# Kernel tuning notes

Measured on AMD Instinct MI355X. Metric: run time of the kernel, lower is better.

## Reference

```python
import math
import jax, jax.numpy as jnp
import numpy as np

B, S, M, H = 8, 2048, 2048, 512
GH = 512  # gate_hidden
MIX_BIAS = -0.25
VARIATION_BIAS = -1.0
PRIOR_SCALE = 1.0
GATE_SCALE = 1.0
GATE_BIAS = 0.0
EPS = 1e-6


def _slerp(a, b, t, eps=EPS):
    # F.normalize semantics: x / max(||x||, eps)
    an = a / jnp.maximum(jnp.linalg.norm(a, axis=-1, keepdims=True), eps)
    bn = b / jnp.maximum(jnp.linalg.norm(b, axis=-1, keepdims=True), eps)
    dot = jnp.clip(jnp.sum(an * bn, axis=-1, keepdims=True), -1.0 + eps, 1.0 - eps)
    omega = jnp.arccos(dot)
    sin_omega = jnp.maximum(jnp.sin(omega), eps)
    t = jnp.clip(t, 0.0, 1.0)
    scale_a = jnp.sin((1.0 - t) * omega) / sin_omega
    scale_b = jnp.sin(t * omega) / sin_omega
    return scale_a * a + scale_b * b


def setup_inputs() -> dict:
    key = jax.random.key(0)
    ks = jax.random.split(key, 20)
    sc = 1.0 / math.sqrt(H)
    sc4 = 1.0 / math.sqrt(4 * H)
    scg = 1.0 / math.sqrt(GH)
    inp = {
        "query": jax.random.normal(ks[0], (B, S, H), jnp.float32),
        "global_anchor": jax.random.normal(ks[1], (B, H), jnp.float32),
        "global_memory": jax.random.normal(ks[2], (B, M, H), jnp.float32),
        "local_absolute": jax.random.normal(ks[3], (B, S, H), jnp.float32),
        "style_context": jax.random.normal(ks[4], (B, S, H), jnp.float32),
        # projection params, stored as [in, out]
        "Wq": jax.random.normal(ks[5], (H, H), jnp.float32) * sc,
        "bq": jnp.zeros((H,), jnp.float32),
        "Wk": jax.random.normal(ks[6], (H, H), jnp.float32) * sc,
        "bk": jnp.zeros((H,), jnp.float32),
        "Wv": jax.random.normal(ks[7], (H, H), jnp.float32) * sc,
        "bv": jnp.zeros((H,), jnp.float32),
        "Wo": jax.random.normal(ks[8], (H, H), jnp.float32) * sc,
        "bo": jnp.zeros((H,), jnp.float32),
        # mix gate MLP: 4H -> GH -> 1
        "Wm1": jax.random.normal(ks[9], (4 * H, GH), jnp.float32) * sc4,
        "bm1": jnp.zeros((GH,), jnp.float32),
        "Wm2": jax.random.normal(ks[10], (GH, 1), jnp.float32) * scg,
        "bm2": jnp.zeros((1,), jnp.float32),
        # variation gate MLP: 4H -> GH -> 1
        "Wg1": jax.random.normal(ks[11], (4 * H, GH), jnp.float32) * sc4,
        "bg1": jnp.zeros((GH,), jnp.float32),
        "Wg2": jax.random.normal(ks[12], (GH, 1), jnp.float32) * scg,
        "bg2": jnp.zeros((1,), jnp.float32),
    }
    return inp


def reference(query, global_anchor, global_memory, local_absolute, style_context,
              Wq, bq, Wk, bk, Wv, bv, Wo, bo,
              Wm1, bm1, Wm2, bm2, Wg1, bg1, Wg2, bg2):
    # expand anchor [B,H] -> [B,S,H]
    anchor_seq = jnp.broadcast_to(global_anchor[:, None, :], query.shape)

    q = query @ Wq + bq                      # [B,S,H]
    k = global_memory @ Wk + bk              # [B,M,H]
    v = global_memory @ Wv + bv              # [B,M,H]

    attn_logits = jnp.einsum('bsh,bmh->bsm', q, k) / math.sqrt(float(H))
    attn = jax.nn.softmax(attn_logits, axis=-1)                      # [B,S,M]
    prior_delta = (jnp.einsum('bsm,bmh->bsh', attn, v) @ Wo + bo) * PRIOR_SCALE
    prior_absolute = anchor_seq + prior_delta

    mix_in = jnp.concatenate([query, prior_absolute, local_absolute, style_context], axis=-1)
    mix_logit = jax.nn.relu(mix_in @ Wm1 + bm1) @ Wm2 + bm2          # [B,S,1]
    mix = jax.nn.sigmoid(mix_logit + MIX_BIAS)

    candidate_absolute = _slerp(prior_absolute, local_absolute, mix)

    var_in = jnp.concatenate([query, candidate_absolute, anchor_seq, style_context], axis=-1)
    variation_logit = jax.nn.relu(var_in @ Wg1 + bg1) @ Wg2 + bg2    # [B,S,1]
    variation_gate = jax.nn.sigmoid(variation_logit * GATE_SCALE + GATE_BIAS + VARIATION_BIAS)

    candidate_delta = candidate_absolute - anchor_seq
    return (attn, prior_delta, prior_absolute, mix, candidate_absolute,
            candidate_delta, variation_logit, variation_gate)
```

## Files before the change

kernel.cpp:

```cpp
#include <hip/hip_runtime.h>
#include <hip/hip_bf16.h>

typedef __hip_bfloat16 bf16;
typedef unsigned short u16;
typedef u16 u16x8 __attribute__((ext_vector_type(8)));
typedef u16 u16x4v __attribute__((ext_vector_type(4)));
typedef short bf16x8 __attribute__((ext_vector_type(8)));
typedef float f32x4 __attribute__((ext_vector_type(4)));

__device__ __forceinline__ float b2f(u16 u) {
    unsigned v = ((unsigned)u) << 16;
    float f; __builtin_memcpy(&f, &v, 4); return f;
}
__device__ __forceinline__ u16 f2u(float f) {
    bf16 h = __float2bfloat16(f);
    u16 u; __builtin_memcpy(&u, &h, 2); return u;
}
__device__ __forceinline__ float sigmoidf_(float x) { return 1.f / (1.f + expf(-x)); }
__device__ __forceinline__ void load8f(const float* __restrict__ p, float* x) {
    float4 a = *reinterpret_cast<const float4*>(p);
    float4 b = *reinterpret_cast<const float4*>(p + 4);
    x[0]=a.x; x[1]=a.y; x[2]=a.z; x[3]=a.w; x[4]=b.x; x[5]=b.y; x[6]=b.z; x[7]=b.w;
}

__device__ __forceinline__ void gld16(const void* g, void* l) {
    typedef __attribute__((address_space(1))) const unsigned int GU;
    typedef __attribute__((address_space(3))) unsigned int LU;
    __builtin_amdgcn_global_load_lds((GU*)(unsigned long long)g,
                                     (LU*)(unsigned int)(unsigned long long)l, 16, 0, 0);
}

template<int EPI, int SWZ>
__global__ __launch_bounds__(256)
void k_mfma(const bf16* __restrict__ A, long long sA, int lda,
            const bf16* __restrict__ Bt, long long sB, int ldb,
            const float* __restrict__ bias,
            bf16* __restrict__ outb, long long sO,
            float* __restrict__ out1, float* __restrict__ out2,
            const float* __restrict__ anchor,
            int N, int K, float scale, int GX)
{
    __shared__ short As[4096];
    __shared__ short Bs[4096];
    const int tid = threadIdx.x;
    const int lin = blockIdx.x;
    int x, y, z;
    if constexpr (SWZ == 0) {
        z = lin & 7; const int t = lin >> 3; x = t % GX; y = t / GX;
    } else {
        const int q = (int)gridDim.x >> 3;
        const int wq = (lin & 7) * q + (lin >> 3);
        x = wq % GX; y = wq / GX; z = 0;
    }
    const int n0 = x * 128, m0 = y * 128;
    const bf16* Az = A + (long long)z * sA;
    const bf16* Bz = Bt + (long long)z * sB;
    const int lrow = tid >> 2;
    const int lcol = (tid & 3) * 8;
    const int lane = tid & 63, w = tid >> 6;
    const int wm = (w >> 1) * 64, wn = (w & 1) * 64;
    const int fr = lane & 15, fq = lane >> 4;
    char* AsW = (char*)As + w * 1024;
    char* BsW = (char*)Bs + w * 1024;

    f32x4 acc[4][4];
#pragma unroll
    for (int i = 0; i < 4; ++i)
#pragma unroll
        for (int j = 0; j < 4; ++j) acc[i][j] = f32x4{0.f, 0.f, 0.f, 0.f};

    for (int k0 = 0; k0 < K; k0 += 32) {
        const bf16* ga = Az + (long long)(m0 + lrow) * lda + (k0 + lcol);
        const bf16* gb = Bz + (long long)(n0 + lrow) * ldb + (k0 + lcol);
        gld16(ga, AsW);
        gld16(ga + 64LL * lda, AsW + 4096);
        gld16(gb, BsW);
        gld16(gb + 64LL * ldb, BsW + 4096);
        __syncthreads();

        bf16x8 af[4], bfr[4];
#pragma unroll
        for (int i = 0; i < 4; ++i)
            af[i] = *reinterpret_cast<const bf16x8*>(&As[(wm + i * 16 + fr) * 32 + fq * 8]);
#pragma unroll
        for (int j = 0; j < 4; ++j)
            bfr[j] = *reinterpret_cast<const bf16x8*>(&Bs[(wn + j * 16 + fr) * 32 + fq * 8]);
#pragma unroll
        for (int i = 0; i < 4; ++i)
#pragma unroll
            for (int j = 0; j < 4; ++j)
                acc[i][j] = __builtin_amdgcn_mfma_f32_16x16x32_bf16(af[i], bfr[j], acc[i][j], 0, 0, 0);
        __syncthreads();
    }

#pragma unroll
    for (int j = 0; j < 4; ++j) {
        const int col = n0 + wn + j * 16 + fr;
        const float bv = bias ? bias[col] : 0.f;
#pragma unroll
        for (int i = 0; i < 4; ++i) {
#pragma unroll
            for (int r = 0; r < 4; ++r) {
                const long long row = m0 + wm + i * 16 + fq * 4 + r;
                const float v = acc[i][j][r];
                if constexpr (EPI == 0) {
                    outb[(long long)z * sO + row * N + col] = __float2bfloat16(v * scale + bv);
                } else {
                    const float pd = v + bv;
                    const float pa = pd + anchor[(row >> 11) * 512 + col];
                    out1[row * N + col] = pd;
                    out2[row * N + col] = pa;
                    outb[row * N + col] = __float2bfloat16(pa);
                }
            }
        }
    }
}

__global__ __launch_bounds__(256)
void k_softmax_b(bf16* __restrict__ Lb, float* __restrict__ attn)
{
    __shared__ float redm[4], reds[4];
    const long long row = blockIdx.x;
    bf16* lp = Lb + row * 2048;
    float* ap = attn + row * 2048;
    const int tid = threadIdx.x;

    u16x8 u = *reinterpret_cast<const u16x8*>(lp + tid * 8);
    float x[8];
    float mx = -1e30f;
#pragma unroll
    for (int j = 0; j < 8; ++j) { x[j] = b2f(u[j]); mx = fmaxf(mx, x[j]); }
#pragma unroll
    for (int off = 32; off; off >>= 1) mx = fmaxf(mx, __shfl_xor(mx, off));
    if ((tid & 63) == 0) redm[tid >> 6] = mx;
    __syncthreads();
    mx = fmaxf(fmaxf(redm[0], redm[1]), fmaxf(redm[2], redm[3]));

    float s = 0.f;
#pragma unroll
    for (int j = 0; j < 8; ++j) { x[j] = __expf(x[j] - mx); s += x[j]; }
#pragma unroll
    for (int off = 32; off; off >>= 1) s += __shfl_xor(s, off);
    if ((tid & 63) == 0) reds[tid >> 6] = s;
    __syncthreads();
    const float inv = 1.f / (reds[0] + reds[1] + reds[2] + reds[3]);

    u16x8 ob;
#pragma unroll
    for (int j = 0; j < 8; ++j) { x[j] *= inv; ob[j] = f2u(x[j]); }
    *reinterpret_cast<float4*>(ap + tid * 8)     = make_float4(x[0], x[1], x[2], x[3]);
    *reinterpret_cast<float4*>(ap + tid * 8 + 4) = make_float4(x[4], x[5], x[6], x[7]);
    *reinterpret_cast<u16x8*>(lp + tid * 8) = ob;
}

__global__ __launch_bounds__(256)
void k_cat(const bf16* __restrict__ s0b, const bf16* __restrict__ s1b,
           const bf16* __restrict__ s2b, const bf16* __restrict__ s3b,
           int mode2,
           const bf16* __restrict__ Bt, const float* __restrict__ bias,
           bf16* __restrict__ outb)
{
    __shared__ short As[4096];
    __shared__ short Bs[4096];
    const int tid = threadIdx.x;
    const int lin = blockIdx.x;
    const int q = (int)gridDim.x >> 3;
    const int wq = (lin & 7) * q + (lin >> 3);
    const int n0 = (wq & 3) * 128, m0 = (wq >> 2) * 128;
    const int lrow = tid >> 2;
    const int lcol = (tid & 3) * 8;
    const int lane = tid & 63, w = tid >> 6;
    const int wm = (w >> 1) * 64, wn = (w & 1) * 64;
    const int fr = lane & 15, fq = lane >> 4;
    char* AsW = (char*)As + w * 1024;
    char* BsW = (char*)Bs + w * 1024;

    f32x4 acc[4][4];
#pragma unroll
    for (int i = 0; i < 4; ++i)
#pragma unroll
        for (int j = 0; j < 4; ++j) acc[i][j] = f32x4{0.f, 0.f, 0.f, 0.f};

    for (int k0 = 0; k0 < 2048; k0 += 32) {
        const int si = k0 >> 9;
        const bf16* sp = si == 0 ? s0b : si == 1 ? s1b : si == 2 ? s2b : s3b;
        const int kloc = (k0 & 511) + lcol;
        const int r = m0 + lrow;
        long long ro0, ro1;
        if (si == 2 && mode2) { ro0 = (long long)(r >> 11) * 512; ro1 = ro0; }
        else                  { ro0 = (long long)r * 512; ro1 = ro0 + 64LL * 512; }
        gld16(sp + ro0 + kloc, AsW);
        gld16(sp + ro1 + kloc, AsW + 4096);
        const bf16* gb = Bt + (long long)(n0 + lrow) * 2048 + (k0 + lcol);
        gld16(gb, BsW);
        gld16(gb + 64LL * 2048, BsW + 4096);
        __syncthreads();

        bf16x8 af[4], bfr[4];
#pragma unroll
        for (int i = 0; i < 4; ++i)
            af[i] = *reinterpret_cast<const bf16x8*>(&As[(wm + i * 16 + fr) * 32 + fq * 8]);
#pragma unroll
        for (int j = 0; j < 4; ++j)
            bfr[j] = *reinterpret_cast<const bf16x8*>(&Bs[(wn + j * 16 + fr) * 32 + fq * 8]);
#pragma unroll
        for (int i = 0; i < 4; ++i)
#pragma unroll
            for (int j = 0; j < 4; ++j)
                acc[i][j] = __builtin_amdgcn_mfma_f32_16x16x32_bf16(af[i], bfr[j], acc[i][j], 0, 0, 0);
        __syncthreads();
    }

#pragma unroll
    for (int j = 0; j < 4; ++j) {
        const int col = n0 + wn + j * 16 + fr;
        const float bv = bias[col];
#pragma unroll
        for (int i = 0; i < 4; ++i)
#pragma unroll
            for (int r = 0; r < 4; ++r) {
                const long long row = m0 + wm + i * 16 + fq * 4 + r;
                outb[row * 512 + col] = __float2bfloat16(fmaxf(acc[i][j][r] + bv, 0.f));
            }
    }
}

__global__ __launch_bounds__(256)
void k_cvt(const float* __restrict__ s, bf16* __restrict__ d, int n)
{
    long long i = ((long long)blockIdx.x * 256 + threadIdx.x) * 8;
    if (i >= n) return;
    float x[8]; load8f(s + i, x);
    u16x8 o;
#pragma unroll
    for (int j = 0; j < 8; ++j) o[j] = f2u(x[j]);
    *reinterpret_cast<u16x8*>(d + i) = o;
}

__global__ __launch_bounds__(256)
void k_tr(const float* s0, bf16* d0, const float* s1, bf16* d1,
          const float* s2, bf16* d2, const float* s3, bf16* d3,
          int R, int C)
{
    __shared__ float t[32][33];
    const int zz = blockIdx.z;
    const float* s = zz == 0 ? s0 : zz == 1 ? s1 : zz == 2 ? s2 : s3;
    bf16* d = zz == 0 ? d0 : zz == 1 ? d1 : zz == 2 ? d2 : d3;
    const int c0 = blockIdx.x * 32, r0 = blockIdx.y * 32;
    const int tr = threadIdx.x >> 3, tc = (threadIdx.x & 7) * 4;
    float4 v = *reinterpret_cast<const float4*>(s + (long long)(r0 + tr) * C + c0 + tc);
    t[tr][tc] = v.x; t[tr][tc + 1] = v.y; t[tr][tc + 2] = v.z; t[tr][tc + 3] = v.w;
    __syncthreads();
    u16x4v o;
    o[0] = f2u(t[tc + 0][tr]); o[1] = f2u(t[tc + 1][tr]);
    o[2] = f2u(t[tc + 2][tr]); o[3] = f2u(t[tc + 3][tr]);
    *reinterpret_cast<u16x4v*>(d + (long long)(c0 + tr) * R + r0 + tc) = o;
}

__global__ __launch_bounds__(256)
void k_trb(const bf16* __restrict__ vb, bf16* __restrict__ vt)
{
    __shared__ u16 t[32][36];
    const int z = blockIdx.z;
    const int h0 = blockIdx.x * 32, s0 = blockIdx.y * 32;
    const int tr = threadIdx.x >> 3, tc = (threadIdx.x & 7) * 4;
    u16x4v a = *reinterpret_cast<const u16x4v*>(
        vb + ((long long)z * 2048 + s0 + tr) * 512 + h0 + tc);
    t[tr][tc] = a[0]; t[tr][tc + 1] = a[1]; t[tr][tc + 2] = a[2]; t[tr][tc + 3] = a[3];
    __syncthreads();
    u16x4v o;
    o[0] = t[tc + 0][tr]; o[1] = t[tc + 1][tr]; o[2] = t[tc + 2][tr]; o[3] = t[tc + 3][tr];
    *reinterpret_cast<u16x4v*>(
        vt + (long long)z * 1048576 + (long long)(h0 + tr) * 2048 + s0 + tc) = o;
}

__global__ __launch_bounds__(64)
void k_gate(const bf16* __restrict__ hidden, const float* __restrict__ w2,
            const float* __restrict__ b2,
            float* __restrict__ outLogit, float* __restrict__ outGate,
            float scl, float add)
{
    const long long row = blockIdx.x;
    const int lane = threadIdx.x;
    u16x8 u = *reinterpret_cast<const u16x8*>(hidden + row * 512 + lane * 8);
    float wv[8];
    load8f(w2 + lane * 8, wv);
    float s = 0.f;
#pragma unroll
    for (int j = 0; j < 8; ++j) s = fmaf(b2f(u[j]), wv[j], s);
#pragma unroll
    for (int off = 32; off; off >>= 1) s += __shfl_xor(s, off);
    if (lane == 0) {
        float logit = s + b2[0];
        if (outLogit) outLogit[row] = logit;
        outGate[row] = sigmoidf_(logit * scl + add);
    }
}

__global__ __launch_bounds__(64)
void k_slerp(const bf16* __restrict__ priorb, const bf16* __restrict__ localb,
             const float* __restrict__ mixv, const float* __restrict__ anchor,
             float* __restrict__ cand, float* __restrict__ cdelta,
             bf16* __restrict__ candb)
{
    const int row = blockIdx.x;
    const int lane = threadIdx.x;
    const long long base = (long long)row * 512 + lane * 8;
    const long long abase = (long long)(row >> 11) * 512 + lane * 8;

    u16x8 ua = *reinterpret_cast<const u16x8*>(priorb + base);
    u16x8 ub = *reinterpret_cast<const u16x8*>(localb + base);
    float a[8], b[8];
    float sa = 0.f, sb = 0.f, sab = 0.f;
#pragma unroll
    for (int j = 0; j < 8; ++j) {
        a[j] = b2f(ua[j]); b[j] = b2f(ub[j]);
        sa = fmaf(a[j], a[j], sa); sb = fmaf(b[j], b[j], sb); sab = fmaf(a[j], b[j], sab);
    }
#pragma unroll
    for (int off = 1; off < 64; off <<= 1) {
        sa += __shfl_xor(sa, off); sb += __shfl_xor(sb, off); sab += __shfl_xor(sab, off);
    }
    const float eps = 1e-6f;
    float na = fmaxf(sqrtf(sa), eps), nb = fmaxf(sqrtf(sb), eps);
    float dot = sab / (na * nb);
    dot = fminf(fmaxf(dot, -1.f + eps), 1.f - eps);
    float omega = acosf(dot);
    float so = fmaxf(sinf(omega), eps);
    float t = mixv[row];
    t = fminf(fmaxf(t, 0.f), 1.f);
    float sca = sinf((1.f - t) * omega) / so;
    float scb = sinf(t * omega) / so;

    float an[8];
    load8f(anchor + abase, an);
    float c0[8], d0[8];
    u16x8 cb;
#pragma unroll
    for (int j = 0; j < 8; ++j) {
        c0[j] = sca * a[j] + scb * b[j];
        d0[j] = c0[j] - an[j];
        cb[j] = f2u(c0[j]);
    }
    *reinterpret_cast<float4*>(cand + base)       = make_float4(c0[0], c0[1], c0[2], c0[3]);
    *reinterpret_cast<float4*>(cand + base + 4)   = make_float4(c0[4], c0[5], c0[6], c0[7]);
    *reinterpret_cast<float4*>(cdelta + base)     = make_float4(d0[0], d0[1], d0[2], d0[3]);
    *reinterpret_cast<float4*>(cdelta + base + 4) = make_float4(d0[4], d0[5], d0[6], d0[7]);
    *reinterpret_cast<u16x8*>(candb + base) = cb;
}

extern "C" void kernel_launch(void* const* d_in, const int* in_sizes, int n_in,
                              void* d_out, int out_size, void* d_ws, size_t ws_size,
                              hipStream_t stream)
{
    const float* query  = (const float*)d_in[0];
    const float* anchor = (const float*)d_in[1];
    const float* gmem   = (const float*)d_in[2];
    const float* local_ = (const float*)d_in[3];
    const float* style  = (const float*)d_in[4];
    const float* Wq = (const float*)d_in[5];   const float* bq = (const float*)d_in[6];
    const float* Wk = (const float*)d_in[7];   const float* bk = (const float*)d_in[8];
    const float* Wv = (const float*)d_in[9];   const float* bv = (const float*)d_in[10];
    const float* Wo = (const float*)d_in[11];  const float* bo = (const float*)d_in[12];
    const float* Wm1 = (const float*)d_in[13]; const float* bm1 = (const float*)d_in[14];
    const float* Wm2 = (const float*)d_in[15]; const float* bm2 = (const float*)d_in[16];
    const float* Wg1 = (const float*)d_in[17]; const float* bg1 = (const float*)d_in[18];
    const float* Wg2 = (const float*)d_in[19]; const float* bg2 = (const float*)d_in[20];

    float* out = (float*)d_out;
    const long long SHE = 8388608LL;
    float* o_attn = out;
    float* o_pd   = out + 33554432LL;
    float* o_pa   = o_pd + SHE;
    float* o_mix  = o_pa + SHE;
    float* o_ca   = o_mix + 16384;
    float* o_cd   = o_ca + SHE;
    float* o_vl   = o_cd + SHE;
    float* o_vg   = o_vl + 16384;

    bf16* S0q = (bf16*)d_ws;
    bf16* S1  = S0q + SHE;
    bf16* S2  = S1 + SHE;
    bf16* S3  = S2 + SHE;
    bf16* S4  = S3 + SHE;
    bf16* wtq = S4 + SHE;
    bf16* wtk = wtq + 262144;
    bf16* wtv = wtk + 262144;
    bf16* wto = wtv + 262144;
    bf16* wtm1 = wto + 262144;
    bf16* wtg1 = wtm1 + 1048576;
    bf16* anb  = wtg1 + 1048576;
    bf16* p_b  = (bf16*)o_ca;
    bf16* v_b  = (bf16*)o_ca;

    const float invSqrtH = 0.04419417382415922f;

    k_cvt<<<4096, 256, 0, stream>>>(query, S0q, 8388608);
    k_cvt<<<4096, 256, 0, stream>>>(gmem, S1, 8388608);
    k_cvt<<<2, 256, 0, stream>>>(anchor, anb, 4096);
    k_tr<<<dim3(16, 16, 4), 256, 0, stream>>>(Wq, wtq, Wk, wtk, Wv, wtv, Wo, wto, 512, 512);
    k_tr<<<dim3(16, 64, 2), 256, 0, stream>>>(Wm1, wtm1, Wg1, wtg1,
                                              nullptr, nullptr, nullptr, nullptr, 2048, 512);
    k_mfma<0, 1><<<512, 256, 0, stream>>>(S0q, 0, 512, wtq, 0, 512, bq,
        S2, 0, nullptr, nullptr, nullptr, 512, 512, 1.f, 4);
    k_mfma<0, 1><<<512, 256, 0, stream>>>(S1, 0, 512, wtk, 0, 512, bk,
        S3, 0, nullptr, nullptr, nullptr, 512, 512, 1.f, 4);
    k_mfma<0, 1><<<512, 256, 0, stream>>>(S1, 0, 512, wtv, 0, 512, bv,
        v_b, 0, nullptr, nullptr, nullptr, 512, 512, 1.f, 4);
    k_trb<<<dim3(16, 64, 8), 256, 0, stream>>>(v_b, S4);
    k_mfma<0, 0><<<2048, 256, 0, stream>>>(S2, 2048LL * 512, 512, S3, 2048LL * 512, 512,
        nullptr, p_b, 4194304LL, nullptr, nullptr, nullptr, 2048, 512, invSqrtH, 16);
    k_softmax_b<<<16384, 256, 0, stream>>>(p_b, o_attn);
    k_mfma<0, 0><<<512, 256, 0, stream>>>(p_b, 4194304LL, 2048, S4, 1048576LL, 2048,
        nullptr, S1, 1048576LL, nullptr, nullptr, nullptr, 512, 2048, 1.f, 4);
    k_cvt<<<4096, 256, 0, stream>>>(local_, S3, 8388608);
    k_cvt<<<4096, 256, 0, stream>>>(style, S4, 8388608);
    k_mfma<2, 1><<<512, 256, 0, stream>>>(S1, 0, 512, wto, 0, 512, bo,
        S2, 0, o_pd, o_pa, anchor, 512, 512, 1.f, 4);
    k_cat<<<512, 256, 0, stream>>>(S0q, S2, S3, S4, 0, wtm1, bm1, S1);
    k_gate<<<16384, 64, 0, stream>>>(S1, Wm2, bm2, nullptr, o_mix, 1.0f, -0.25f);
    k_slerp<<<16384, 64, 0, stream>>>(S2, S3, o_mix, anchor, o_ca, o_cd, S2);
    k_cat<<<512, 256, 0, stream>>>(S0q, S2, anb, S4, 1, wtg1, bg1, S1);
    k_gate<<<16384, 64, 0, stream>>>(S1, Wg2, bg2, o_vl, o_vg, 1.0f, -1.0f);
}
```

Before: 459.4 us.

## Fuse gate second layer into cat GEMM epilogue and merge prologue kernels

The gate MLP's second layer (dot with w2) now runs in the k_cat GEMM epilogue, which writes per-column-tile partial sums instead of a bf16 hidden tensor. The slerp kernel folds the mix-gate reduction into itself, and a small kernel finishes the variation gate. The K and V projections are merged into one wider GEMM, and the conversion and transpose prologue kernels become a single launch. This removes hidden-tensor writes and reads plus several launches, at the cost of shuffle reductions in the epilogue and a summation order that differs from the original.

```diff
diff --git a/kernel.cpp b/kernel.cpp
--- a/kernel.cpp
+++ b/kernel.cpp
@@ -34,8 +34,8 @@
 __global__ __launch_bounds__(256)
 void k_mfma(const bf16* __restrict__ A, long long sA, int lda,
             const bf16* __restrict__ Bt, long long sB, int ldb,
-            const float* __restrict__ bias,
-            bf16* __restrict__ outb, long long sO,
+            const float* __restrict__ bias, const float* __restrict__ bias2,
+            bf16* __restrict__ outb, bf16* __restrict__ outb2, long long sO,
             float* __restrict__ out1, float* __restrict__ out2,
             const float* __restrict__ anchor,
             int N, int K, float scale, int GX)
@@ -96,7 +96,9 @@
 #pragma unroll
     for (int j = 0; j < 4; ++j) {
         const int col = n0 + wn + j * 16 + fr;
-        const float bv = bias ? bias[col] : 0.f;
+        float bv;
+        if constexpr (EPI == 1) bv = (col < 512) ? bias[col] : bias2[col - 512];
+        else                    bv = bias ? bias[col] : 0.f;
 #pragma unroll
         for (int i = 0; i < 4; ++i) {
 #pragma unroll
@@ -105,6 +107,9 @@
                 const float v = acc[i][j][r];
                 if constexpr (EPI == 0) {
                     outb[(long long)z * sO + row * N + col] = __float2bfloat16(v * scale + bv);
+                } else if constexpr (EPI == 1) {
+                    if (col < 512) outb[row * 512 + col] = __float2bfloat16(v + bv);
+                    else           outb2[row * 512 + (col - 512)] = __float2bfloat16(v + bv);
                 } else {
                     const float pd = v + bv;
                     const float pa = pd + anchor[(row >> 11) * 512 + col];
@@ -159,15 +164,17 @@
            const bf16* __restrict__ s2b, const bf16* __restrict__ s3b,
            int mode2,
            const bf16* __restrict__ Bt, const float* __restrict__ bias,
-           bf16* __restrict__ outb)
+           const float* __restrict__ w2, float* __restrict__ part)
 {
     __shared__ short As[4096];
     __shared__ short Bs[4096];
+    __shared__ float pl[128][2];
     const int tid = threadIdx.x;
     const int lin = blockIdx.x;
     const int q = (int)gridDim.x >> 3;
     const int wq = (lin & 7) * q + (lin >> 3);
-    const int n0 = (wq & 3) * 128, m0 = (wq >> 2) * 128;
+    const int xt = wq & 3;
+    const int n0 = xt * 128, m0 = (wq >> 2) * 128;
     const int lrow = tid >> 2;
     const int lcol = (tid & 3) * 8;
     const int lane = tid & 63, w = tid >> 6;
@@ -212,50 +219,108 @@
         __syncthreads();
     }
 
+    float pt[4][4];
+#pragma unroll
+    for (int i = 0; i < 4; ++i)
+#pragma unroll
+        for (int r = 0; r < 4; ++r) pt[i][r] = 0.f;
 #pragma unroll
     for (int j = 0; j < 4; ++j) {
         const int col = n0 + wn + j * 16 + fr;
         const float bv = bias[col];
-#pragma unroll
-        for (int i = 0; i < 4; ++i)
-#pragma unroll
-            for (int r = 0; r < 4; ++r) {
-                const long long row = m0 + wm + i * 16 + fq * 4 + r;
-                outb[row * 512 + col] = __float2bfloat16(fmaxf(acc[i][j][r] + bv, 0.f));
-            }
-    }
-}
-
-__global__ __launch_bounds__(256)
-void k_cvt(const float* __restrict__ s, bf16* __restrict__ d, int n)
-{
-    long long i = ((long long)blockIdx.x * 256 + threadIdx.x) * 8;
-    if (i >= n) return;
+        const float wv = w2[col];
+#pragma unroll
+        for (int i = 0; i < 4; ++i)
+#pragma unroll
+            for (int r = 0; r < 4; ++r)
+                pt[i][r] = fmaf(fmaxf(acc[i][j][r] + bv, 0.f), wv, pt[i][r]);
+    }
+#pragma unroll
+    for (int off = 1; off < 16; off <<= 1)
+#pragma unroll
+        for (int i = 0; i < 4; ++i)
+#pragma unroll
+            for (int r = 0; r < 4; ++r)
+                pt[i][r] += __shfl_xor(pt[i][r], off);
+    if (fr == 0)
+#pragma unroll
+        for (int i = 0; i < 4; ++i)
+#pragma unroll
+            for (int r = 0; r < 4; ++r)
+                pl[wm + i * 16 + fq * 4 + r][wn >> 6] = pt[i][r];
+    __syncthreads();
+    if (tid < 128)
+        part[(long long)(m0 + tid) * 4 + xt] = pl[tid][0] + pl[tid][1];
+}
+
+__global__ __launch_bounds__(256)
+void k_prologue(const float* __restrict__ query, bf16* __restrict__ qb,
+                const float* __restrict__ gmem, bf16* __restrict__ gb,
+                const float* __restrict__ anchor, bf16* __restrict__ anb,
+                const float* Wq, bf16* wtq, const float* Wk, bf16* wtk,
+                const float* Wv, bf16* wtv, const float* Wo, bf16* wto,
+                const float* Wm1, bf16* wtm1, const float* Wg1, bf16* wtg1)
+{
+    __shared__ float tls[32][33];
+    const int b = blockIdx.x;
+    const int tid = threadIdx.x;
+    if (b < 8192) {
+        const float* s = (b < 4096) ? query : gmem;
+        bf16* d = (b < 4096) ? qb : gb;
+        const long long i = ((long long)(b & 4095) * 256 + tid) * 8;
+        float x[8]; load8f(s + i, x);
+        u16x8 o;
+#pragma unroll
+        for (int j = 0; j < 8; ++j) o[j] = f2u(x[j]);
+        *reinterpret_cast<u16x8*>(d + i) = o;
+        return;
+    }
+    if (b < 8194) {
+        const int i = ((b - 8192) * 256 + tid) * 8;
+        if (i < 4096) {
+            float x[8]; load8f(anchor + i, x);
+            u16x8 o;
+#pragma unroll
+            for (int j = 0; j < 8; ++j) o[j] = f2u(x[j]);
+            *reinterpret_cast<u16x8*>(anb + i) = o;
+        }
+        return;
+    }
+    const float* s; bf16* d; int R, C, ti;
+    if (b < 9218) {
+        const int bi = b - 8194; const int zz = bi >> 8; ti = bi & 255;
+        s = zz == 0 ? Wq : zz == 1 ? Wk : zz == 2 ? Wv : Wo;
+        d = zz == 0 ? wtq : zz == 1 ? wtk : zz == 2 ? wtv : wto;
+        R = 512; C = 512;
+    } else {
+        const int bi = b - 9218; const int zz = bi >> 10; ti = bi & 1023;
+        s = zz ? Wg1 : Wm1; d = zz ? wtg1 : wtm1;
+        R = 2048; C = 512;
+    }
+    const int c0 = (ti & 15) * 32, r0 = (ti >> 4) * 32;
+    const int tr = tid >> 3, tc = (tid & 7) * 4;
+    float4 v = *reinterpret_cast<const float4*>(s + (long long)(r0 + tr) * C + c0 + tc);
+    tls[tr][tc] = v.x; tls[tr][tc + 1] = v.y; tls[tr][tc + 2] = v.z; tls[tr][tc + 3] = v.w;
+    __syncthreads();
+    u16x4v o;
+    o[0] = f2u(tls[tc + 0][tr]); o[1] = f2u(tls[tc + 1][tr]);
+    o[2] = f2u(tls[tc + 2][tr]); o[3] = f2u(tls[tc + 3][tr]);
+    *reinterpret_cast<u16x4v*>(d + (long long)(c0 + tr) * R + r0 + tc) = o;
+}
+
+__global__ __launch_bounds__(256)
+void k_cvt2(const float* __restrict__ s0, bf16* __restrict__ d0,
+            const float* __restrict__ s1, bf16* __restrict__ d1)
+{
+    const int b = blockIdx.x;
+    const float* s = (b < 4096) ? s0 : s1;
+    bf16* d = (b < 4096) ? d0 : d1;
+    const long long i = ((long long)(b & 4095) * 256 + threadIdx.x) * 8;
     float x[8]; load8f(s + i, x);
     u16x8 o;
 #pragma unroll
     for (int j = 0; j < 8; ++j) o[j] = f2u(x[j]);
     *reinterpret_cast<u16x8*>(d + i) = o;
-}
-
-__global__ __launch_bounds__(256)
-void k_tr(const float* s0, bf16* d0, const float* s1, bf16* d1,
-          const float* s2, bf16* d2, const float* s3, bf16* d3,
-          int R, int C)
-{
-    __shared__ float t[32][33];
-    const int zz = blockIdx.z;
-    const float* s = zz == 0 ? s0 : zz == 1 ? s1 : zz == 2 ? s2 : s3;
-    bf16* d = zz == 0 ? d0 : zz == 1 ? d1 : zz == 2 ? d2 : d3;
-    const int c0 = blockIdx.x * 32, r0 = blockIdx.y * 32;
-    const int tr = threadIdx.x >> 3, tc = (threadIdx.x & 7) * 4;
-    float4 v = *reinterpret_cast<const float4*>(s + (long long)(r0 + tr) * C + c0 + tc);
-    t[tr][tc] = v.x; t[tr][tc + 1] = v.y; t[tr][tc + 2] = v.z; t[tr][tc + 3] = v.w;
-    __syncthreads();
-    u16x4v o;
-    o[0] = f2u(t[tc + 0][tr]); o[1] = f2u(t[tc + 1][tr]);
-    o[2] = f2u(t[tc + 2][tr]); o[3] = f2u(t[tc + 3][tr]);
-    *reinterpret_cast<u16x4v*>(d + (long long)(c0 + tr) * R + r0 + tc) = o;
 }
 
 __global__ __launch_bounds__(256)
@@ -276,39 +341,25 @@
 }
 
 __global__ __launch_bounds__(64)
-void k_gate(const bf16* __restrict__ hidden, const float* __restrict__ w2,
-            const float* __restrict__ b2,
-            float* __restrict__ outLogit, float* __restrict__ outGate,
-            float scl, float add)
-{
-    const long long row = blockIdx.x;
-    const int lane = threadIdx.x;
-    u16x8 u = *reinterpret_cast<const u16x8*>(hidden + row * 512 + lane * 8);
-    float wv[8];
-    load8f(w2 + lane * 8, wv);
-    float s = 0.f;
-#pragma unroll
-    for (int j = 0; j < 8; ++j) s = fmaf(b2f(u[j]), wv[j], s);
-#pragma unroll
-    for (int off = 32; off; off >>= 1) s += __shfl_xor(s, off);
-    if (lane == 0) {
-        float logit = s + b2[0];
-        if (outLogit) outLogit[row] = logit;
-        outGate[row] = sigmoidf_(logit * scl + add);
-    }
-}
-
-__global__ __launch_bounds__(64)
-void k_slerp(const bf16* __restrict__ priorb, const bf16* __restrict__ localb,
-             const float* __restrict__ mixv, const float* __restrict__ anchor,
-             float* __restrict__ cand, float* __restrict__ cdelta,
-             bf16* __restrict__ candb)
+void k_gate_slerp(const float* __restrict__ part, const float* __restrict__ b2,
+                  const bf16* __restrict__ priorb, const bf16* __restrict__ localb,
+                  const float* __restrict__ anchor,
+                  float* __restrict__ o_mix,
+                  float* __restrict__ cand, float* __restrict__ cdelta,
+                  bf16* __restrict__ candb)
 {
     const int row = blockIdx.x;
     const int lane = threadIdx.x;
+    float v = (lane < 4) ? part[(long long)row * 4 + lane] : 0.f;
+    v += __shfl_xor(v, 1);
+    v += __shfl_xor(v, 2);
+    const float logit = __shfl(v, 0) + b2[0];
+    float t = sigmoidf_(logit - 0.25f);
+    if (lane == 0) o_mix[row] = t;
+    t = fminf(fmaxf(t, 0.f), 1.f);
+
     const long long base = (long long)row * 512 + lane * 8;
     const long long abase = (long long)(row >> 11) * 512 + lane * 8;
-
     u16x8 ua = *reinterpret_cast<const u16x8*>(priorb + base);
     u16x8 ub = *reinterpret_cast<const u16x8*>(localb + base);
     float a[8], b[8];
@@ -328,8 +379,6 @@
     dot = fminf(fmaxf(dot, -1.f + eps), 1.f - eps);
     float omega = acosf(dot);
     float so = fmaxf(sinf(omega), eps);
-    float t = mixv[row];
-    t = fminf(fmaxf(t, 0.f), 1.f);
     float sca = sinf((1.f - t) * omega) / so;
     float scb = sinf(t * omega) / so;
 
@@ -348,6 +397,17 @@
     *reinterpret_cast<float4*>(cdelta + base)     = make_float4(d0[0], d0[1], d0[2], d0[3]);
     *reinterpret_cast<float4*>(cdelta + base + 4) = make_float4(d0[4], d0[5], d0[6], d0[7]);
     *reinterpret_cast<u16x8*>(candb + base) = cb;
+}
+
+__global__ __launch_bounds__(256)
+void k_gate_var(const float* __restrict__ part, const float* __restrict__ b2,
+                float* __restrict__ o_vl, float* __restrict__ o_vg)
+{
+    const long long row = (long long)blockIdx.x * 256 + threadIdx.x;
+    float4 p = *reinterpret_cast<const float4*>(part + row * 4);
+    const float logit = (p.x + p.y) + (p.z + p.w) + b2[0];
+    o_vl[row] = logit;
+    o_vg[row] = sigmoidf_(logit - 1.0f);
 }
 
 extern "C" void kernel_launch(void* const* d_in, const int* in_sizes, int n_in,
@@ -391,36 +451,33 @@
     bf16* wtm1 = wto + 262144;
     bf16* wtg1 = wtm1 + 1048576;
     bf16* anb  = wtg1 + 1048576;
+    float* part_m = (float*)(anb + 4096);
+    float* part_v = part_m + 65536;
     bf16* p_b  = (bf16*)o_ca;
     bf16* v_b  = (bf16*)o_ca;
 
     const float invSqrtH = 0.04419417382415922f;
 
-    k_cvt<<<4096, 256, 0, stream>>>(query, S0q, 8388608);
-    k_cvt<<<4096, 256, 0, stream>>>(gmem, S1, 8388608);
-    k_cvt<<<2, 256, 0, stream>>>(anchor, anb, 4096);
-    k_tr<<<dim3(16, 16, 4), 256, 0, stream>>>(Wq, wtq, Wk, wtk, Wv, wtv, Wo, wto, 512, 512);
-    k_tr<<<dim3(16, 64, 2), 256, 0, stream>>>(Wm1, wtm1, Wg1, wtg1,
-                                              nullptr, nullptr, nullptr, nullptr, 2048, 512);
-    k_mfma<0, 1><<<512, 256, 0, stream>>>(S0q, 0, 512, wtq, 0, 512, bq,
-        S2, 0, nullptr, nullptr, nullptr, 512, 512, 1.f, 4);
-    k_mfma<0, 1><<<512, 256, 0, stream>>>(S1, 0, 512, wtk, 0, 512, bk,
-        S3, 0, nullptr, nullptr, nullptr, 512, 512, 1.f, 4);
-    k_mfma<0, 1><<<512, 256, 0, stream>>>(S1, 0, 512, wtv, 0, 512, bv,
-        v_b, 0, nullptr, nullptr, nullptr, 512, 512, 1.f, 4);
+    k_prologue<<<11266, 256, 0, stream>>>(query, S0q, gmem, S1, anchor, anb,
+        Wq, wtq, Wk, wtk, Wv, wtv, Wo, wto, Wm1, wtm1, Wg1, wtg1);
+    k_mfma<0, 1><<<512, 256, 0, stream>>>(S0q, 0, 512, wtq, 0, 512, bq, nullptr,
+        S2, nullptr, 0, nullptr, nullptr, nullptr, 512, 512, 1.f, 4);
+    k_mfma<1, 1><<<1024, 256, 0, stream>>>(S1, 0, 512, wtk, 0, 512, bk, bv,
+        S3, v_b, 0, nullptr, nullptr, nullptr, 1024, 512, 1.f, 8);
     k_trb<<<dim3(16, 64, 8), 256, 0, stream>>>(v_b, S4);
     k_mfma<0, 0><<<2048, 256, 0, stream>>>(S2, 2048LL * 512, 512, S3, 2048LL * 512, 512,
-        nullptr, p_b, 4194304LL, nullptr, nullptr, nullptr, 2048, 512, invSqrtH, 16);
+        nullptr, nullptr, p_b, nullptr, 4194304LL, nullptr, nullptr, nullptr,
+        2048, 512, invSqrtH, 16);
     k_softmax_b<<<16384, 256, 0, stream>>>(p_b, o_attn);
     k_mfma<0, 0><<<512, 256, 0, stream>>>(p_b, 4194304LL, 2048, S4, 1048576LL, 2048,
-        nullptr, S1, 1048576LL, nullptr, nullptr, nullptr, 512, 2048, 1.f, 4);
-    k_cvt<<<4096, 256, 0, stream>>>(local_, S3, 8388608);
-    k_cvt<<<4096, 256, 0, stream>>>(style, S4, 8388608);
-    k_mfma<2, 1><<<512, 256, 0, stream>>>(S1, 0, 512, wto, 0, 512, bo,
-        S2, 0, o_pd, o_pa, anchor, 512, 512, 1.f, 4);
-    k_cat<<<512, 256, 0, stream>>>(S0q, S2, S3, S4, 0, wtm1, bm1, S1);
-    k_gate<<<16384, 64, 0, stream>>>(S1, Wm2, bm2, nullptr, o_mix, 1.0f, -0.25f);
-    k_slerp<<<16384, 64, 0, stream>>>(S2, S3, o_mix, anchor, o_ca, o_cd, S2);
-    k_cat<<<512, 256, 0, stream>>>(S0q, S2, anb, S4, 1, wtg1, bg1, S1);
-    k_gate<<<16384, 64, 0, stream>>>(S1, Wg2, bg2, o_vl, o_vg, 1.0f, -1.0f);
-}
+        nullptr, nullptr, S1, nullptr, 1048576LL, nullptr, nullptr, nullptr,
+        512, 2048, 1.f, 4);
+    k_cvt2<<<8192, 256, 0, stream>>>(local_, S3, style, S4);
+    k_mfma<2, 1><<<512, 256, 0, stream>>>(S1, 0, 512, wto, 0, 512, bo, nullptr,
+        S2, nullptr, 0, o_pd, o_pa, anchor, 512, 512, 1.f, 4);
+    k_cat<<<512, 256, 0, stream>>>(S0q, S2, S3, S4, 0, wtm1, bm1, Wm2, part_m);
+    k_gate_slerp<<<16384, 64, 0, stream>>>(part_m, bm2, S2, S3, anchor,
+        o_mix, o_ca, o_cd, S2);
+    k_cat<<<512, 256, 0, stream>>>(S0q, S2, anb, S4, 1, wtg1, bg1, Wg2, part_v);
+    k_gate_var<<<64, 256, 0, stream>>>(part_v, bg2, o_vl, o_vg);
+}
```

New measurement: 430.8 us. 1.07x faster.
